# Performance work log

Hardware: AMD Instinct MI355X
Metric: run time of the kernel (lower is better)

The kernel has to match this reference:

```python
import jax, jax.numpy as jnp
import numpy as np

N_NODES = 100000
IN_DIM = 64
OUT_DIM = 64
N_EDGES = 1250000


def setup_inputs() -> dict:
    key = jax.random.key(0)
    k1, k2, k3, k4 = jax.random.split(key, 4)
    x = jax.random.normal(k1, (N_NODES, IN_DIM), dtype=jnp.float32)
    edge_index = jax.random.randint(k2, (2, N_EDGES), 0, N_NODES, dtype=jnp.int32)
    # Linear weights stored as [in, out] so y = x @ W (equivalent to torch x @ W.T)
    s = 1.0 / np.sqrt(IN_DIM)
    W1 = jax.random.uniform(k3, (IN_DIM, OUT_DIM), dtype=jnp.float32, minval=-s, maxval=s)
    W2 = jax.random.uniform(k4, (IN_DIM, OUT_DIM), dtype=jnp.float32, minval=-s, maxval=s)
    return {"x": x, "edge_index": edge_index, "W1": W1, "W2": W2}


def reference(x, edge_index, W1, W2):
    # self part: [N, out]
    self_part = x @ W1
    # transform-then-gather is mathematically identical to gather-then-transform
    # (linear map commutes with row gather) and cheaper when E > N.
    msgs = (x @ W2)[edge_index[0]]            # [E, out]
    neighbor_part = jax.ops.segment_sum(msgs, edge_index[1], num_segments=x.shape[0])
    return jax.nn.relu(self_part + neighbor_part)
```

## Files before the change

### kernel.cpp

```cpp
#include <hip/hip_runtime.h>

#define N_NODES 100000
#define N_EDGES 1250000
#define DIM 64

#define B_SHIFT 7
#define BUCKET_NODES 128
#define NBUCKETS ((N_NODES + BUCKET_NODES - 1) / BUCKET_NODES)
#define CAP 2560
#define CHUNK 2048
#define NBLK_EDGE ((N_EDGES + CHUNK - 1) / CHUNK)
#define GEMM_BLOCKS 1024
#define SG_THREADS 512

typedef __attribute__((ext_vector_type(8))) short short8;
typedef __attribute__((ext_vector_type(4))) float f32x4;

static __host__ __device__ inline size_t align256(size_t x) { return (x + 255) & ~(size_t)255; }

__device__ inline float bf16_to_f32(unsigned short u) {
  return __uint_as_float(((unsigned)u) << 16);
}
__device__ inline unsigned short f32_to_bf16(float f) {
  unsigned u = __float_as_uint(f);
  u += 0x7FFFu + ((u >> 16) & 1u);
  return (unsigned short)(u >> 16);
}

__global__ __launch_bounds__(256) void partition_edges(
    const int* __restrict__ ei,
    int* __restrict__ gcursor,
    unsigned* __restrict__ pairs) {
  __shared__ int h[NBUCKETS];
  __shared__ int gbase[NBUCKETS];
  const int nE = N_EDGES;

  for (int i = threadIdx.x; i < NBUCKETS; i += 256) h[i] = 0;
  __syncthreads();
  int base = blockIdx.x * CHUNK;
  int end = min(base + CHUNK, nE);
  for (int e = base + (int)threadIdx.x; e < end; e += 256)
    atomicAdd(&h[ei[nE + e] >> B_SHIFT], 1);
  __syncthreads();
  for (int i = threadIdx.x; i < NBUCKETS; i += 256) {
    int c = h[i];
    gbase[i] = c ? atomicAdd(&gcursor[i], c) : 0;
    h[i] = 0;
  }
  __syncthreads();
  for (int e = base + (int)threadIdx.x; e < end; e += 256) {
    int dst = ei[nE + e];
    int src = ei[e];
    int b = dst >> B_SHIFT;
    int pos = gbase[b] + atomicAdd(&h[b], 1);
    if (pos < CAP)
      pairs[b * CAP + pos] = (unsigned)src | ((unsigned)(dst & (BUCKET_NODES - 1)) << 17);
  }
}

__global__ __launch_bounds__(256) void gemm_mfma(
    const float* __restrict__ x,
    const float* __restrict__ W1,
    const float* __restrict__ W2,
    unsigned short* __restrict__ y1b,
    unsigned short* __restrict__ y2b,
    int nTiles) {
  int lane = threadIdx.x & 63;
  int wave = (blockIdx.x * 256 + (int)threadIdx.x) >> 6;
  int nWaves = GEMM_BLOCKS * 4;
  int m = lane & 15;
  int q = lane >> 4;

  short8 wf[2][2][4];
#pragma unroll
  for (int w = 0; w < 2; ++w) {
    const float* W = w ? W2 : W1;
#pragma unroll
    for (int kh = 0; kh < 2; ++kh)
#pragma unroll
      for (int nt = 0; nt < 4; ++nt) {
        short8 f;
#pragma unroll
        for (int j = 0; j < 8; ++j) {
          int k = kh * 32 + q * 8 + j;
          f[j] = (short)f32_to_bf16(W[k * DIM + nt * 16 + m]);
        }
        wf[w][kh][nt] = f;
      }
  }

  for (int t = wave; t < nTiles; t += nWaves) {
    int rowBase = t * 16;
    const float* xr = x + (size_t)(rowBase + m) * DIM + q * 8;

    short8 af[2];
#pragma unroll
    for (int kh = 0; kh < 2; ++kh) {
      float4 u0 = *(const float4*)(xr + kh * 32);
      float4 u1 = *(const float4*)(xr + kh * 32 + 4);
      short8 f;
      f[0] = (short)f32_to_bf16(u0.x);
      f[1] = (short)f32_to_bf16(u0.y);
      f[2] = (short)f32_to_bf16(u0.z);
      f[3] = (short)f32_to_bf16(u0.w);
      f[4] = (short)f32_to_bf16(u1.x);
      f[5] = (short)f32_to_bf16(u1.y);
      f[6] = (short)f32_to_bf16(u1.z);
      f[7] = (short)f32_to_bf16(u1.w);
      af[kh] = f;
    }

#pragma unroll
    for (int w = 0; w < 2; ++w) {
      unsigned short* Y = w ? y2b : y1b;
      f32x4 acc[4];
#pragma unroll
      for (int nt = 0; nt < 4; ++nt) {
        acc[nt] = (f32x4){0.f, 0.f, 0.f, 0.f};
        acc[nt] = __builtin_amdgcn_mfma_f32_16x16x32_bf16(af[0], wf[w][0][nt], acc[nt], 0, 0, 0);
        acc[nt] = __builtin_amdgcn_mfma_f32_16x16x32_bf16(af[1], wf[w][1][nt], acc[nt], 0, 0, 0);
      }
#pragma unroll
      for (int nt = 0; nt < 4; ++nt)
#pragma unroll
        for (int r = 0; r < 4; ++r)
          Y[(size_t)(rowBase + q * 4 + r) * DIM + nt * 16 + m] = f32_to_bf16(acc[nt][r]);
    }
  }
}

__global__ __launch_bounds__(SG_THREADS) void sort_gather(
    const unsigned* __restrict__ pairs,
    const int* __restrict__ gcursor,
    const unsigned short* __restrict__ y1b,
    const unsigned short* __restrict__ y2b,
    float* __restrict__ out,
    int nNodesTotal) {
  __shared__ unsigned buf[CAP];
  __shared__ unsigned sorted[CAP];
  __shared__ int cnt[BUCKET_NODES];
  __shared__ int scn[BUCKET_NODES];
  __shared__ int cur[BUCKET_NODES];

  int b = blockIdx.x;
  int n = min(gcursor[b], CAP);
  int tid = threadIdx.x;
  const unsigned* pb = pairs + (size_t)b * CAP;

  if (tid < BUCKET_NODES) cnt[tid] = 0;
  __syncthreads();
  for (int i = tid; i < n; i += SG_THREADS) {
    unsigned w = pb[i];
    buf[i] = w;
    atomicAdd(&cnt[(w >> 17) & 127], 1);
  }
  __syncthreads();

  int v = 0;
  if (tid < BUCKET_NODES) { v = cnt[tid]; scn[tid] = v; }
  __syncthreads();
#pragma unroll
  for (int off = 1; off < BUCKET_NODES; off <<= 1) {
    int t = 0;
    if (tid < BUCKET_NODES && tid >= off) t = scn[tid - off];
    __syncthreads();
    if (tid < BUCKET_NODES) scn[tid] += t;
    __syncthreads();
  }
  if (tid < BUCKET_NODES) cur[tid] = scn[tid] - v;
  __syncthreads();

  for (int i = tid; i < n; i += SG_THREADS) {
    unsigned w = buf[i];
    int l = (int)((w >> 17) & 127);
    int p = atomicAdd(&cur[l], 1);
    sorted[p] = w & 0x1FFFFu;
  }
  __syncthreads();

  int lane = tid & 63;
  int wv = tid >> 6;
  int c = lane & 31;
  int hh = lane >> 5;
  const ushort2* y2v = (const ushort2*)y2b;
  const ushort2* y1v = (const ushort2*)y1b;
  int nodeBase = b << B_SHIFT;
  int numNodes = min(BUCKET_NODES, nNodesTotal - nodeBase);

  for (int ln = wv; ln < numNodes; ln += (SG_THREADS / 64)) {
    int deg = cnt[ln];
    int begin = scn[ln] - deg;
    int end = begin + deg;

    float ax0 = 0.f, ay0 = 0.f, ax1 = 0.f, ay1 = 0.f;
    float bx0 = 0.f, by0 = 0.f, bx1 = 0.f, by1 = 0.f;
    int e = begin;
    for (; e + 7 < end; e += 8) {
      int s0 = (int)sorted[e + hh];
      int s1 = (int)sorted[e + 2 + hh];
      int s2 = (int)sorted[e + 4 + hh];
      int s3 = (int)sorted[e + 6 + hh];
      ushort2 u0 = y2v[(size_t)s0 * 32 + c];
      ushort2 u1 = y2v[(size_t)s1 * 32 + c];
      ushort2 u2 = y2v[(size_t)s2 * 32 + c];
      ushort2 u3 = y2v[(size_t)s3 * 32 + c];
      ax0 += bf16_to_f32(u0.x); ay0 += bf16_to_f32(u0.y);
      ax1 += bf16_to_f32(u1.x); ay1 += bf16_to_f32(u1.y);
      bx0 += bf16_to_f32(u2.x); by0 += bf16_to_f32(u2.y);
      bx1 += bf16_to_f32(u3.x); by1 += bf16_to_f32(u3.y);
    }
    for (; e + 3 < end; e += 4) {
      int s0 = (int)sorted[e + hh];
      int s1 = (int)sorted[e + 2 + hh];
      ushort2 u0 = y2v[(size_t)s0 * 32 + c];
      ushort2 u1 = y2v[(size_t)s1 * 32 + c];
      ax0 += bf16_to_f32(u0.x); ay0 += bf16_to_f32(u0.y);
      ax1 += bf16_to_f32(u1.x); ay1 += bf16_to_f32(u1.y);
    }
    for (; e < end; e += 2) {
      int ee = e + hh;
      if (ee < end) {
        int s = (int)sorted[ee];
        ushort2 u = y2v[(size_t)s * 32 + c];
        ax0 += bf16_to_f32(u.x); ay0 += bf16_to_f32(u.y);
      }
    }

    float sx = (ax0 + ax1) + (bx0 + bx1);
    float sy = (ay0 + ay1) + (by0 + by1);
    sx += __shfl_xor(sx, 32, 64);
    sy += __shfl_xor(sy, 32, 64);

    if (lane < 32) {
      int node = nodeBase + ln;
      ushort2 s1v = y1v[(size_t)node * 32 + c];
      float2* ov = (float2*)out;
      float2 o;
      o.x = fmaxf(bf16_to_f32(s1v.x) + sx, 0.0f);
      o.y = fmaxf(bf16_to_f32(s1v.y) + sy, 0.0f);
      ov[(size_t)node * 32 + c] = o;
    }
  }
}

__global__ __launch_bounds__(256) void gemm_simple(
    const float* __restrict__ x, const float* __restrict__ W1, const float* __restrict__ W2,
    float* __restrict__ y1, unsigned short* __restrict__ y2b, int n) {
  int row = blockIdx.x * blockDim.x + threadIdx.x;
  if (row >= n) return;
  float xv[DIM];
  const float4* xr = (const float4*)(x + (size_t)row * DIM);
#pragma unroll
  for (int i = 0; i < DIM / 4; ++i) {
    float4 t = xr[i];
    xv[4 * i] = t.x; xv[4 * i + 1] = t.y; xv[4 * i + 2] = t.z; xv[4 * i + 3] = t.w;
  }
#pragma unroll
  for (int m = 0; m < 2; ++m) {
    const float* W = (m == 0) ? W1 : W2;
#pragma unroll
    for (int cc = 0; cc < DIM; cc += 16) {
      float acc[16];
#pragma unroll
      for (int c2 = 0; c2 < 16; ++c2) acc[c2] = 0.0f;
      for (int k = 0; k < DIM; ++k) {
        float xk = xv[k];
        const float* wr = W + k * DIM + cc;
#pragma unroll
        for (int c2 = 0; c2 < 16; ++c2) acc[c2] = fmaf(xk, wr[c2], acc[c2]);
      }
      if (m == 0) {
        for (int c2 = 0; c2 < 16; ++c2) y1[(size_t)row * DIM + cc + c2] = acc[c2];
      } else {
        for (int c2 = 0; c2 < 16; ++c2) y2b[(size_t)row * DIM + cc + c2] = f32_to_bf16(acc[c2]);
      }
    }
  }
}

__global__ __launch_bounds__(256) void scatter_add(const int* __restrict__ ei,
                                                   const unsigned short* __restrict__ y2b,
                                                   float* __restrict__ out, int nE) {
  int gid = blockIdx.x * blockDim.x + threadIdx.x;
  int edge = gid >> 6;
  int lane = threadIdx.x & 63;
  if (edge >= nE) return;
  int src = __builtin_amdgcn_readfirstlane(ei[edge]);
  int dst = __builtin_amdgcn_readfirstlane(ei[nE + edge]);
  atomicAdd(&out[(size_t)dst * DIM + lane], bf16_to_f32(y2b[(size_t)src * DIM + lane]));
}

__global__ __launch_bounds__(256) void relu_inplace(float* __restrict__ out, int n4) {
  int i = blockIdx.x * blockDim.x + threadIdx.x;
  if (i >= n4) return;
  float4* p = (float4*)out;
  float4 v = p[i];
  v.x = fmaxf(v.x, 0.0f);
  v.y = fmaxf(v.y, 0.0f);
  v.z = fmaxf(v.z, 0.0f);
  v.w = fmaxf(v.w, 0.0f);
  p[i] = v;
}

extern "C" void kernel_launch(void* const* d_in, const int* in_sizes, int n_in,
                              void* d_out, int out_size, void* d_ws, size_t ws_size,
                              hipStream_t stream) {
  const float* x  = (const float*)d_in[0];
  const int*   ei = (const int*)d_in[1];
  const float* W1 = (const float*)d_in[2];
  const float* W2 = (const float*)d_in[3];
  float* out = (float*)d_out;

  char* ws = (char*)d_ws;
  size_t off = 0;
  unsigned short* y2b = (unsigned short*)(ws + off); off += align256((size_t)N_NODES * DIM * sizeof(unsigned short));
  unsigned short* y1b = (unsigned short*)(ws + off); off += align256((size_t)N_NODES * DIM * sizeof(unsigned short));
  int* gcursor = (int*)(ws + off);                   off += align256((size_t)NBUCKETS * sizeof(int));
  unsigned* pairs = (unsigned*)(ws + off);           off += align256((size_t)NBUCKETS * CAP * sizeof(unsigned));
  size_t required = off;

  if (ws_size >= required) {
    hipMemsetAsync(gcursor, 0, (size_t)NBUCKETS * sizeof(int), stream);
    partition_edges<<<NBLK_EDGE, 256, 0, stream>>>(ei, gcursor, pairs);
    gemm_mfma<<<GEMM_BLOCKS, 256, 0, stream>>>(x, W1, W2, y1b, y2b, N_NODES / 16);
    sort_gather<<<NBUCKETS, SG_THREADS, 0, stream>>>(pairs, gcursor, y1b, y2b, out, N_NODES);
  } else {
    {
      int blocks = (N_NODES + 255) / 256;
      gemm_simple<<<blocks, 256, 0, stream>>>(x, W1, W2, out, y2b, N_NODES);
    }
    {
      long long threads = (long long)N_EDGES * 64;
      int blocks = (int)((threads + 255) / 256);
      scatter_add<<<blocks, 256, 0, stream>>>(ei, y2b, out, N_EDGES);
    }
    {
      int n4 = N_NODES * DIM / 4;
      int blocks = (n4 + 255) / 256;
      relu_inplace<<<blocks, 256, 0, stream>>>(out, n4);
    }
  }
}
```

Baseline: 159.1 us.

## Fuse edge partition with GEMM launch and widen gather loads to ushort4

```diff
diff --git a/kernel.cpp b/kernel.cpp
--- a/kernel.cpp
+++ b/kernel.cpp
@@ -10,8 +10,8 @@
 #define CAP 2560
 #define CHUNK 2048
 #define NBLK_EDGE ((N_EDGES + CHUNK - 1) / CHUNK)
-#define GEMM_BLOCKS 1024
-#define SG_THREADS 512
+#define GEMM_BLOCKS 512
+#define SG_THREADS 1024
 
 typedef __attribute__((ext_vector_type(8))) short short8;
 typedef __attribute__((ext_vector_type(4))) float f32x4;
@@ -27,104 +27,104 @@
   return (unsigned short)(u >> 16);
 }
 
-__global__ __launch_bounds__(256) void partition_edges(
-    const int* __restrict__ ei,
-    int* __restrict__ gcursor,
-    unsigned* __restrict__ pairs) {
-  __shared__ int h[NBUCKETS];
-  __shared__ int gbase[NBUCKETS];
-  const int nE = N_EDGES;
-
-  for (int i = threadIdx.x; i < NBUCKETS; i += 256) h[i] = 0;
-  __syncthreads();
-  int base = blockIdx.x * CHUNK;
-  int end = min(base + CHUNK, nE);
-  for (int e = base + (int)threadIdx.x; e < end; e += 256)
-    atomicAdd(&h[ei[nE + e] >> B_SHIFT], 1);
-  __syncthreads();
-  for (int i = threadIdx.x; i < NBUCKETS; i += 256) {
-    int c = h[i];
-    gbase[i] = c ? atomicAdd(&gcursor[i], c) : 0;
-    h[i] = 0;
-  }
-  __syncthreads();
-  for (int e = base + (int)threadIdx.x; e < end; e += 256) {
-    int dst = ei[nE + e];
-    int src = ei[e];
-    int b = dst >> B_SHIFT;
-    int pos = gbase[b] + atomicAdd(&h[b], 1);
-    if (pos < CAP)
-      pairs[b * CAP + pos] = (unsigned)src | ((unsigned)(dst & (BUCKET_NODES - 1)) << 17);
-  }
-}
-
-__global__ __launch_bounds__(256) void gemm_mfma(
+__global__ __launch_bounds__(256) void fused_gemm_partition(
     const float* __restrict__ x,
     const float* __restrict__ W1,
     const float* __restrict__ W2,
     unsigned short* __restrict__ y1b,
     unsigned short* __restrict__ y2b,
+    const int* __restrict__ ei,
+    int* __restrict__ gcursor,
+    unsigned* __restrict__ pairs,
     int nTiles) {
-  int lane = threadIdx.x & 63;
-  int wave = (blockIdx.x * 256 + (int)threadIdx.x) >> 6;
-  int nWaves = GEMM_BLOCKS * 4;
-  int m = lane & 15;
-  int q = lane >> 4;
-
-  short8 wf[2][2][4];
-#pragma unroll
-  for (int w = 0; w < 2; ++w) {
-    const float* W = w ? W2 : W1;
-#pragma unroll
-    for (int kh = 0; kh < 2; ++kh)
-#pragma unroll
-      for (int nt = 0; nt < 4; ++nt) {
+  __shared__ int h[NBUCKETS];
+  __shared__ int gbase[NBUCKETS];
+
+  if (blockIdx.x < NBLK_EDGE) {
+    const int nE = N_EDGES;
+    for (int i = threadIdx.x; i < NBUCKETS; i += 256) h[i] = 0;
+    __syncthreads();
+    int base = blockIdx.x * CHUNK;
+    int end = min(base + CHUNK, nE);
+    for (int e = base + (int)threadIdx.x; e < end; e += 256)
+      atomicAdd(&h[ei[nE + e] >> B_SHIFT], 1);
+    __syncthreads();
+    for (int i = threadIdx.x; i < NBUCKETS; i += 256) {
+      int c = h[i];
+      gbase[i] = c ? atomicAdd(&gcursor[i], c) : 0;
+      h[i] = 0;
+    }
+    __syncthreads();
+    for (int e = base + (int)threadIdx.x; e < end; e += 256) {
+      int dst = ei[nE + e];
+      int src = ei[e];
+      int b = dst >> B_SHIFT;
+      int pos = gbase[b] + atomicAdd(&h[b], 1);
+      if (pos < CAP)
+        pairs[b * CAP + pos] = (unsigned)src | ((unsigned)(dst & (BUCKET_NODES - 1)) << 17);
+    }
+  } else {
+    int lane = threadIdx.x & 63;
+    int wave = ((blockIdx.x - NBLK_EDGE) * 256 + (int)threadIdx.x) >> 6;
+    int nWaves = GEMM_BLOCKS * 4;
+    int m = lane & 15;
+    int q = lane >> 4;
+
+    short8 wf[2][2][4];
+#pragma unroll
+    for (int w = 0; w < 2; ++w) {
+      const float* W = w ? W2 : W1;
+#pragma unroll
+      for (int kh = 0; kh < 2; ++kh)
+#pragma unroll
+        for (int nt = 0; nt < 4; ++nt) {
+          short8 f;
+#pragma unroll
+          for (int j = 0; j < 8; ++j) {
+            int k = kh * 32 + q * 8 + j;
+            f[j] = (short)f32_to_bf16(W[k * DIM + nt * 16 + m]);
+          }
+          wf[w][kh][nt] = f;
+        }
+    }
+
+    for (int t = wave; t < nTiles; t += nWaves) {
+      int rowBase = t * 16;
+      const float* xr = x + (size_t)(rowBase + m) * DIM + q * 8;
+
+      short8 af[2];
+#pragma unroll
+      for (int kh = 0; kh < 2; ++kh) {
+        float4 u0 = *(const float4*)(xr + kh * 32);
+        float4 u1 = *(const float4*)(xr + kh * 32 + 4);
         short8 f;
-#pragma unroll
-        for (int j = 0; j < 8; ++j) {
-          int k = kh * 32 + q * 8 + j;
-          f[j] = (short)f32_to_bf16(W[k * DIM + nt * 16 + m]);
+        f[0] = (short)f32_to_bf16(u0.x);
+        f[1] = (short)f32_to_bf16(u0.y);
+        f[2] = (short)f32_to_bf16(u0.z);
+        f[3] = (short)f32_to_bf16(u0.w);
+        f[4] = (short)f32_to_bf16(u1.x);
+        f[5] = (short)f32_to_bf16(u1.y);
+        f[6] = (short)f32_to_bf16(u1.z);
+        f[7] = (short)f32_to_bf16(u1.w);
+        af[kh] = f;
+      }
+
+#pragma unroll
+      for (int w = 0; w < 2; ++w) {
+        unsigned short* Y = w ? y2b : y1b;
+        f32x4 acc[4];
+#pragma unroll
+        for (int nt = 0; nt < 4; ++nt) {
+          acc[nt] = (f32x4){0.f, 0.f, 0.f, 0.f};
+          acc[nt] = __builtin_amdgcn_mfma_f32_16x16x32_bf16(af[0], wf[w][0][nt], acc[nt], 0, 0, 0);
+          acc[nt] = __builtin_amdgcn_mfma_f32_16x16x32_bf16(af[1], wf[w][1][nt], acc[nt], 0, 0, 0);
         }
-        wf[w][kh][nt] = f;
+#pragma unroll
+        for (int nt = 0; nt < 4; ++nt)
+#pragma unroll
+          for (int r = 0; r < 4; ++r)
+            Y[(size_t)(rowBase + q * 4 + r) * DIM + nt * 16 + m] = f32_to_bf16(acc[nt][r]);
       }
-  }
-
-  for (int t = wave; t < nTiles; t += nWaves) {
-    int rowBase = t * 16;
-    const float* xr = x + (size_t)(rowBase + m) * DIM + q * 8;
-
-    short8 af[2];
-#pragma unroll
-    for (int kh = 0; kh < 2; ++kh) {
-      float4 u0 = *(const float4*)(xr + kh * 32);
-      float4 u1 = *(const float4*)(xr + kh * 32 + 4);
-      short8 f;
-      f[0] = (short)f32_to_bf16(u0.x);
-      f[1] = (short)f32_to_bf16(u0.y);
-      f[2] = (short)f32_to_bf16(u0.z);
-      f[3] = (short)f32_to_bf16(u0.w);
-      f[4] = (short)f32_to_bf16(u1.x);
-      f[5] = (short)f32_to_bf16(u1.y);
-      f[6] = (short)f32_to_bf16(u1.z);
-      f[7] = (short)f32_to_bf16(u1.w);
-      af[kh] = f;
-    }
-
-#pragma unroll
-    for (int w = 0; w < 2; ++w) {
-      unsigned short* Y = w ? y2b : y1b;
-      f32x4 acc[4];
-#pragma unroll
-      for (int nt = 0; nt < 4; ++nt) {
-        acc[nt] = (f32x4){0.f, 0.f, 0.f, 0.f};
-        acc[nt] = __builtin_amdgcn_mfma_f32_16x16x32_bf16(af[0], wf[w][0][nt], acc[nt], 0, 0, 0);
-        acc[nt] = __builtin_amdgcn_mfma_f32_16x16x32_bf16(af[1], wf[w][1][nt], acc[nt], 0, 0, 0);
-      }
-#pragma unroll
-      for (int nt = 0; nt < 4; ++nt)
-#pragma unroll
-        for (int r = 0; r < 4; ++r)
-          Y[(size_t)(rowBase + q * 4 + r) * DIM + nt * 16 + m] = f32_to_bf16(acc[nt][r]);
     }
   }
 }
@@ -180,10 +180,10 @@
 
   int lane = tid & 63;
   int wv = tid >> 6;
-  int c = lane & 31;
-  int hh = lane >> 5;
-  const ushort2* y2v = (const ushort2*)y2b;
-  const ushort2* y1v = (const ushort2*)y1b;
+  int g = lane >> 4;
+  int c16 = lane & 15;
+  const ushort4* y2q = (const ushort4*)y2b;
+  const ushort4* y1q = (const ushort4*)y1b;
   int nodeBase = b << B_SHIFT;
   int numNodes = min(BUCKET_NODES, nNodesTotal - nodeBase);
 
@@ -192,53 +192,51 @@
     int begin = scn[ln] - deg;
     int end = begin + deg;
 
-    float ax0 = 0.f, ay0 = 0.f, ax1 = 0.f, ay1 = 0.f;
-    float bx0 = 0.f, by0 = 0.f, bx1 = 0.f, by1 = 0.f;
+    float ax = 0.f, ay = 0.f, az = 0.f, aw = 0.f;
+    float bx = 0.f, by = 0.f, bz = 0.f, bw = 0.f;
     int e = begin;
     for (; e + 7 < end; e += 8) {
-      int s0 = (int)sorted[e + hh];
-      int s1 = (int)sorted[e + 2 + hh];
-      int s2 = (int)sorted[e + 4 + hh];
-      int s3 = (int)sorted[e + 6 + hh];
-      ushort2 u0 = y2v[(size_t)s0 * 32 + c];
-      ushort2 u1 = y2v[(size_t)s1 * 32 + c];
-      ushort2 u2 = y2v[(size_t)s2 * 32 + c];
-      ushort2 u3 = y2v[(size_t)s3 * 32 + c];
-      ax0 += bf16_to_f32(u0.x); ay0 += bf16_to_f32(u0.y);
-      ax1 += bf16_to_f32(u1.x); ay1 += bf16_to_f32(u1.y);
-      bx0 += bf16_to_f32(u2.x); by0 += bf16_to_f32(u2.y);
-      bx1 += bf16_to_f32(u3.x); by1 += bf16_to_f32(u3.y);
+      int s0 = (int)sorted[e + g];
+      int s1 = (int)sorted[e + 4 + g];
+      ushort4 u0 = y2q[(size_t)s0 * 16 + c16];
+      ushort4 u1 = y2q[(size_t)s1 * 16 + c16];
+      ax += bf16_to_f32(u0.x); ay += bf16_to_f32(u0.y);
+      az += bf16_to_f32(u0.z); aw += bf16_to_f32(u0.w);
+      bx += bf16_to_f32(u1.x); by += bf16_to_f32(u1.y);
+      bz += bf16_to_f32(u1.z); bw += bf16_to_f32(u1.w);
     }
     for (; e + 3 < end; e += 4) {
-      int s0 = (int)sorted[e + hh];
-      int s1 = (int)sorted[e + 2 + hh];
-      ushort2 u0 = y2v[(size_t)s0 * 32 + c];
-      ushort2 u1 = y2v[(size_t)s1 * 32 + c];
-      ax0 += bf16_to_f32(u0.x); ay0 += bf16_to_f32(u0.y);
-      ax1 += bf16_to_f32(u1.x); ay1 += bf16_to_f32(u1.y);
-    }
-    for (; e < end; e += 2) {
-      int ee = e + hh;
-      if (ee < end) {
-        int s = (int)sorted[ee];
-        ushort2 u = y2v[(size_t)s * 32 + c];
-        ax0 += bf16_to_f32(u.x); ay0 += bf16_to_f32(u.y);
-      }
-    }
-
-    float sx = (ax0 + ax1) + (bx0 + bx1);
-    float sy = (ay0 + ay1) + (by0 + by1);
+      int s = (int)sorted[e + g];
+      ushort4 u = y2q[(size_t)s * 16 + c16];
+      ax += bf16_to_f32(u.x); ay += bf16_to_f32(u.y);
+      az += bf16_to_f32(u.z); aw += bf16_to_f32(u.w);
+    }
+    if (e + g < end) {
+      int s = (int)sorted[e + g];
+      ushort4 u = y2q[(size_t)s * 16 + c16];
+      ax += bf16_to_f32(u.x); ay += bf16_to_f32(u.y);
+      az += bf16_to_f32(u.z); aw += bf16_to_f32(u.w);
+    }
+
+    float sx = ax + bx, sy = ay + by, sz = az + bz, sw = aw + bw;
+    sx += __shfl_xor(sx, 16, 64);
+    sy += __shfl_xor(sy, 16, 64);
+    sz += __shfl_xor(sz, 16, 64);
+    sw += __shfl_xor(sw, 16, 64);
     sx += __shfl_xor(sx, 32, 64);
     sy += __shfl_xor(sy, 32, 64);
-
-    if (lane < 32) {
+    sz += __shfl_xor(sz, 32, 64);
+    sw += __shfl_xor(sw, 32, 64);
+
+    if (lane < 16) {
       int node = nodeBase + ln;
-      ushort2 s1v = y1v[(size_t)node * 32 + c];
-      float2* ov = (float2*)out;
-      float2 o;
+      ushort4 s1v = y1q[(size_t)node * 16 + lane];
+      float4 o;
       o.x = fmaxf(bf16_to_f32(s1v.x) + sx, 0.0f);
       o.y = fmaxf(bf16_to_f32(s1v.y) + sy, 0.0f);
-      ov[(size_t)node * 32 + c] = o;
+      o.z = fmaxf(bf16_to_f32(s1v.z) + sz, 0.0f);
+      o.w = fmaxf(bf16_to_f32(s1v.w) + sw, 0.0f);
+      ((float4*)out)[(size_t)node * 16 + lane] = o;
     }
   }
 }
@@ -321,8 +319,8 @@
 
   if (ws_size >= required) {
     hipMemsetAsync(gcursor, 0, (size_t)NBUCKETS * sizeof(int), stream);
-    partition_edges<<<NBLK_EDGE, 256, 0, stream>>>(ei, gcursor, pairs);
-    gemm_mfma<<<GEMM_BLOCKS, 256, 0, stream>>>(x, W1, W2, y1b, y2b, N_NODES / 16);
+    fused_gemm_partition<<<NBLK_EDGE + GEMM_BLOCKS, 256, 0, stream>>>(
+        x, W1, W2, y1b, y2b, ei, gcursor, pairs, N_NODES / 16);
     sort_gather<<<NBUCKETS, SG_THREADS, 0, stream>>>(pairs, gcursor, y1b, y2b, out, N_NODES);
   } else {
     {
```

Result: no change. 157.8 us (-0.8%).
